# Performance work log

Hardware: AMD Instinct MI355X
Metric: run time of the kernel (lower is better)

Reference implementation:

```python
import jax, jax.numpy as jnp
import numpy as np

G, N, F_IN = 1024, 256, 128
HID = [256, 256, 256]
KS = [32, 16, 8]
N_OUT = 2


def _graph_conv(adj, x, W, b, act):
    # DGL GraphConv, norm='both': h = D^{-1/2} A D^{-1/2} X W + b
    deg = adj.sum(-1)                                   # [G, n]
    norm = jax.lax.rsqrt(jnp.maximum(deg, 1.0))[..., None]
    h = (x * norm) @ W                                  # [G, n, d_out]
    h = jnp.einsum('gnm,gmd->gnd', adj, h) * norm + b
    return act(h) if act is not None else h


def _sag_pool(adj, x, Ws, bs, k):
    # SAGPool: score via GraphConv, keep top-k nodes, gate by tanh(score),
    # take induced subgraph adjacency.
    score = _graph_conv(adj, x, Ws, bs, None)[..., 0]   # [G, n]
    sv, idx = jax.lax.top_k(score, k)                   # [G, k]
    x_sel = jnp.take_along_axis(x, idx[:, :, None], axis=1) * jnp.tanh(sv)[:, :, None]
    a = jnp.take_along_axis(adj, idx[:, :, None], axis=1)
    a = jnp.take_along_axis(a, idx[:, None, :], axis=2)  # [G, k, k]
    return a, x_sel


def _sum_max_readout(x):
    return jnp.concatenate([x.sum(axis=1), x.max(axis=1)], axis=-1)  # [G, 2d]


def setup_inputs() -> dict:
    key = jax.random.key(0)
    ks = jax.random.split(key, 16)
    feat = jax.random.normal(ks[0], (G, N, F_IN), dtype=jnp.float32)
    # sparse-ish symmetric binary adjacency, avg degree ~ 16
    a = (jax.random.uniform(ks[1], (G, N, N)) < (16.0 / N)).astype(jnp.float32)
    adj = jnp.maximum(a, jnp.swapaxes(a, 1, 2))

    def glorot(k, shp):
        lim = float(np.sqrt(6.0 / (shp[0] + shp[1])))
        return jax.random.uniform(k, shp, jnp.float32, -lim, lim)

    dims = [F_IN] + HID
    inp = {'feat': feat, 'adj': adj}
    for i in range(3):
        inp[f'W{i}'] = glorot(ks[2 + i], (dims[i], dims[i + 1]))
        inp[f'b{i}'] = jnp.zeros((dims[i + 1],), jnp.float32)
        inp[f'Ws{i}'] = glorot(ks[5 + i], (dims[i + 1], 1))
        inp[f'bs{i}'] = jnp.zeros((1,), jnp.float32)
    inp['Wd1'] = glorot(ks[8], (2 * sum(HID), 128))
    inp['bd1'] = jnp.zeros((128,), jnp.float32)
    inp['Wd2'] = glorot(ks[9], (128, N_OUT))
    inp['bd2'] = jnp.zeros((N_OUT,), jnp.float32)
    return inp


def reference(feat, adj, W0, b0, Ws0, bs0, W1, b1, Ws1, bs1, W2, b2, Ws2, bs2,
              Wd1, bd1, Wd2, bd2):
    act = jax.nn.leaky_relu  # F.leaky_relu, slope 0.01
    Wgs = [(W0, b0), (W1, b1), (W2, b2)]
    Wss = [(Ws0, bs0), (Ws1, bs1), (Ws2, bs2)]
    readouts = []
    x, a = feat, adj
    for i in range(3):
        x = _graph_conv(a, x, Wgs[i][0], Wgs[i][1], act)
        a, x = _sag_pool(a, x, Wss[i][0], Wss[i][1], KS[i])
        readouts.append(_sum_max_readout(x))
    merged = jnp.concatenate(readouts, axis=1)          # [G, 2*sum(HID)]
    # dropout omitted (deterministic eval reference)
    h = act(merged @ Wd1 + bd1)
    out = jax.nn.sigmoid(h @ Wd2 + bd2)                 # [G, n_output]
    return out
```

## Files before the change

kernel.cpp:

```cpp
#include <hip/hip_runtime.h>
#include <math.h>

constexpr int GG  = 1024;
constexpr int NN  = 256;
constexpr int FF  = 128;
constexpr int DD  = 256;
constexpr int KS0 = 32, KS1 = 16, KS2 = 8;

__device__ __forceinline__ float lrelu(float x){ return x >= 0.f ? x : 0.01f*x; }

__device__ __forceinline__ unsigned short f2bf(float f) {
  unsigned u = __float_as_uint(f);
  unsigned r = (u + 0x7FFFu + ((u >> 16) & 1u)) >> 16;
  return (unsigned short)r;
}
__device__ __forceinline__ float bf2f(unsigned short h) {
  return __uint_as_float(((unsigned)h) << 16);
}

typedef __attribute__((ext_vector_type(8)))  __bf16 bf16x8;
typedef __attribute__((ext_vector_type(16))) float  f32x16;

union Frag8 { unsigned short us[8]; unsigned long long u64[2]; bf16x8 v; };

__global__ void k_splitW(const float* __restrict__ W, unsigned short* __restrict__ out, int K) {
  int e = blockIdx.x*256 + threadIdx.x;
  if (e >= DD*K) return;
  int j    = e & 7;
  int lane = (e >> 3) & 63;
  int nt   = (e >> 9) & 7;
  int s    = (e >> 12) & 1;
  int kti  = e >> 13;
  int n = nt*32 + (lane & 31);
  int k = kti*32 + s*16 + ((lane >> 5) << 3) + j;
  float x = W[(size_t)k*DD + n];
  unsigned short h1 = f2bf(x);  float r1 = x - bf2f(h1);
  unsigned short h2 = f2bf(r1); float r2 = r1 - bf2f(h2);
  unsigned short h3 = f2bf(r2);
  out[e] = h1; out[DD*K + e] = h2; out[2*DD*K + e] = h3;
}

__global__ void k_maskrow(const float* __restrict__ adj, float* __restrict__ norm0,
                          unsigned long long* __restrict__ mask) {
  int row = blockIdx.x*4 + (threadIdx.x >> 6);
  int lane = threadIdx.x & 63;
  const float* ar = adj + (size_t)row*NN;
  float f0 = ar[lane], f1 = ar[64 + lane], f2 = ar[128 + lane], f3 = ar[192 + lane];
  unsigned long long m0 = __ballot(f0 > 0.5f);
  unsigned long long m1 = __ballot(f1 > 0.5f);
  unsigned long long m2 = __ballot(f2 > 0.5f);
  unsigned long long m3 = __ballot(f3 > 0.5f);
  if (lane < 4) {
    unsigned long long mm = lane == 0 ? m0 : lane == 1 ? m1 : lane == 2 ? m2 : m3;
    mask[(size_t)row*4 + lane] = mm;
  }
  if (lane == 0) {
    int cnt = __popcll(m0) + __popcll(m1) + __popcll(m2) + __popcll(m3);
    norm0[row] = rsqrtf(fmaxf((float)cnt, 1.0f));
  }
}

constexpr int QS = 68;
__global__ __launch_bounds__(256, 2) void k_spmm_f(
    const float* __restrict__ feat, const unsigned long long* __restrict__ mask,
    const float* __restrict__ norm0, float* __restrict__ T0) {
  __shared__ unsigned short ls[3*128*QS];
  __shared__ float snorm[NN];

  int g = blockIdx.x;
  int t = threadIdx.x;
  int lane = t & 63, wave = t >> 6;
  int lm = lane & 31, lh = lane >> 5;

  const float* Xg = feat + (size_t)g*NN*FF;

  snorm[t] = norm0[g*NN + t];

  unsigned long long mrow[2][4];
  #pragma unroll
  for (int mt = 0; mt < 2; ++mt) {
    const unsigned long long* mp = mask + ((size_t)g*NN + wave*64 + mt*32 + lm)*4;
    #pragma unroll
    for (int w = 0; w < 4; ++w) mrow[mt][w] = mp[w];
  }

  f32x16 acc[2][4];
  #pragma unroll
  for (int i = 0; i < 2; ++i)
    #pragma unroll
    for (int j = 0; j < 4; ++j) acc[i][j] = (f32x16)0.0f;

  __syncthreads();

  for (int kq = 0; kq < 4; ++kq) {
    #pragma unroll
    for (int i = 0; i < 8; ++i) {
      int g2 = t + i*256;
      int c  = g2 & 127;
      int mg = g2 >> 7;
      int m0 = kq*64 + mg*4;
      unsigned long long p1 = 0, p2 = 0, p3 = 0;
      #pragma unroll
      for (int jj = 0; jj < 4; ++jj) {
        float x = Xg[(size_t)(m0 + jj)*FF + c] * snorm[m0 + jj];
        unsigned short h1 = f2bf(x);  float r1 = x - bf2f(h1);
        unsigned short h2 = f2bf(r1); float r2 = r1 - bf2f(h2);
        unsigned short h3 = f2bf(r2);
        p1 |= (unsigned long long)h1 << (16*jj);
        p2 |= (unsigned long long)h2 << (16*jj);
        p3 |= (unsigned long long)h3 << (16*jj);
      }
      int base = c*QS + mg*4;
      *reinterpret_cast<unsigned long long*>(&ls[base])            = p1;
      *reinterpret_cast<unsigned long long*>(&ls[128*QS + base])   = p2;
      *reinterpret_cast<unsigned long long*>(&ls[2*128*QS + base]) = p3;
    }
    __syncthreads();

    #pragma unroll
    for (int ktq = 0; ktq < 2; ++ktq) {
      Frag8 afr[2][2];
      #pragma unroll
      for (int mt = 0; mt < 2; ++mt)
        #pragma unroll
        for (int s = 0; s < 2; ++s) {
          int shift = ktq*32 + s*16 + lh*8;
          unsigned byte = (unsigned)(mrow[mt][kq] >> shift) & 0xFFu;
          #pragma unroll
          for (int j = 0; j < 8; ++j)
            afr[mt][s].us[j] = ((byte >> j) & 1u) ? (unsigned short)0x3F80 : (unsigned short)0;
        }
      #pragma unroll
      for (int s = 0; s < 2; ++s)
        #pragma unroll
        for (int nt = 0; nt < 4; ++nt) {
          int kk = ktq*32 + s*16 + lh*8;
          int base = (nt*32 + lm)*QS + kk;
          Frag8 b0_, b1_, b2_;
          b0_.v = *reinterpret_cast<const bf16x8*>(&ls[base]);
          b1_.v = *reinterpret_cast<const bf16x8*>(&ls[128*QS + base]);
          b2_.v = *reinterpret_cast<const bf16x8*>(&ls[2*128*QS + base]);
          #pragma unroll
          for (int mt = 0; mt < 2; ++mt) {
            acc[mt][nt] = __builtin_amdgcn_mfma_f32_32x32x16_bf16(afr[mt][s].v, b0_.v, acc[mt][nt], 0,0,0);
            acc[mt][nt] = __builtin_amdgcn_mfma_f32_32x32x16_bf16(afr[mt][s].v, b1_.v, acc[mt][nt], 0,0,0);
            acc[mt][nt] = __builtin_amdgcn_mfma_f32_32x32x16_bf16(afr[mt][s].v, b2_.v, acc[mt][nt], 0,0,0);
          }
        }
    }
    __syncthreads();
  }

  #pragma unroll
  for (int mt = 0; mt < 2; ++mt)
    #pragma unroll
    for (int nt = 0; nt < 4; ++nt)
      #pragma unroll
      for (int r = 0; r < 16; ++r) {
        int row = wave*64 + mt*32 + (r & 3) + 8*(r >> 2) + 4*lh;
        int col = nt*32 + lm;
        T0[((size_t)g*NN + row)*FF + col] = acc[mt][nt][r];
      }
}

__global__ __launch_bounds__(256, 2) void k_gemm0(
    const float* __restrict__ Tmat, const unsigned short* __restrict__ Wk,
    const float* __restrict__ normv, const float* __restrict__ bias,
    const float* __restrict__ Ws, float* __restrict__ hs) {
  __shared__ unsigned short bsh[3*8192];
  int t = threadIdx.x;
  int lane = t & 63, wave = t >> 6;
  int lm = lane & 31, lh = lane >> 5;
  int rowbase = blockIdx.x*128 + wave*32;

  f32x16 acc[8];
  #pragma unroll
  for (int nt = 0; nt < 8; ++nt) acc[nt] = (f32x16)0.0f;

  for (int kti = 0; kti < 4; ++kti) {
    int kt = kti*32;
    float4 af[2][2];
    #pragma unroll
    for (int s = 0; s < 2; ++s) {
      const float* ap = Tmat + (size_t)(rowbase + lm)*FF + kt + s*16 + lh*8;
      af[s][0] = *reinterpret_cast<const float4*>(ap);
      af[s][1] = *reinterpret_cast<const float4*>(ap + 4);
    }
    __syncthreads();
    #pragma unroll
    for (int sp = 0; sp < 3; ++sp)
      #pragma unroll
      for (int r = 0; r < 4; ++r) {
        const uint4* src = reinterpret_cast<const uint4*>(
            Wk + (size_t)sp*DD*FF + (size_t)kti*8192 + r*2048 + t*8);
        *reinterpret_cast<uint4*>(bsh + sp*8192 + r*2048 + t*8) = *src;
      }
    __syncthreads();
    Frag8 afr[2][3];
    #pragma unroll
    for (int s = 0; s < 2; ++s) {
      const float* fv = &af[s][0].x;
      #pragma unroll
      for (int j = 0; j < 8; ++j) {
        float x = fv[j];
        unsigned short h1 = f2bf(x);  float r1 = x - bf2f(h1);
        unsigned short h2 = f2bf(r1); float r2 = r1 - bf2f(h2);
        afr[s][0].us[j] = h1; afr[s][1].us[j] = h2; afr[s][2].us[j] = f2bf(r2);
      }
    }
    #pragma unroll
    for (int s = 0; s < 2; ++s)
      #pragma unroll
      for (int nt = 0; nt < 8; ++nt) {
        const unsigned short* bp = bsh + ((s*8 + nt)*64 + lane)*8;
        Frag8 b0_, b1_, b2_;
        b0_.v = *reinterpret_cast<const bf16x8*>(bp);
        b1_.v = *reinterpret_cast<const bf16x8*>(bp + 8192);
        b2_.v = *reinterpret_cast<const bf16x8*>(bp + 16384);
        acc[nt] = __builtin_amdgcn_mfma_f32_32x32x16_bf16(afr[s][0].v, b0_.v, acc[nt], 0,0,0);
        acc[nt] = __builtin_amdgcn_mfma_f32_32x32x16_bf16(afr[s][0].v, b1_.v, acc[nt], 0,0,0);
        acc[nt] = __builtin_amdgcn_mfma_f32_32x32x16_bf16(afr[s][1].v, b0_.v, acc[nt], 0,0,0);
        acc[nt] = __builtin_amdgcn_mfma_f32_32x32x16_bf16(afr[s][0].v, b2_.v, acc[nt], 0,0,0);
        acc[nt] = __builtin_amdgcn_mfma_f32_32x32x16_bf16(afr[s][2].v, b0_.v, acc[nt], 0,0,0);
        acc[nt] = __builtin_amdgcn_mfma_f32_32x32x16_bf16(afr[s][1].v, b1_.v, acc[nt], 0,0,0);
      }
  }

  float bcol[8], wcol[8];
  #pragma unroll
  for (int nt = 0; nt < 8; ++nt) { int col = nt*32 + lm; bcol[nt] = bias[col]; wcol[nt] = Ws[col]; }
  float hsum[16];
  #pragma unroll
  for (int r = 0; r < 16; ++r) {
    int row = rowbase + (r & 3) + 8*(r >> 2) + 4*lh;
    float nv = normv[row];
    float hp = 0.f;
    #pragma unroll
    for (int nt = 0; nt < 8; ++nt) hp += lrelu(nv*acc[nt][r] + bcol[nt])*wcol[nt];
    hsum[r] = hp;
  }
  #pragma unroll
  for (int off = 1; off <= 16; off <<= 1)
    #pragma unroll
    for (int r = 0; r < 16; ++r) hsum[r] += __shfl_xor(hsum[r], off);
  if (lm == 0)
    #pragma unroll
    for (int r = 0; r < 16; ++r) {
      int row = rowbase + (r & 3) + 8*(r >> 2) + 4*lh;
      hs[row] = normv[row]*hsum[r];
    }
}

template<int K, bool WRITE_X>
__global__ __launch_bounds__(64, 2) void k_gemm_mfma(
    const float* __restrict__ Tmat, const unsigned short* __restrict__ Wk,
    const float* __restrict__ normv, const float* __restrict__ bias,
    const float* __restrict__ Ws, float* __restrict__ xout, float* __restrict__ hs) {
  int lane = threadIdx.x;
  int lm = lane & 31, lh = lane >> 5;
  int rowbase = blockIdx.x * 32;

  f32x16 acc[8];
  #pragma unroll
  for (int nt = 0; nt < 8; ++nt) acc[nt] = (f32x16)0.0f;

  for (int kt = 0; kt < K; kt += 32) {
    float4 af[2][2];
    #pragma unroll
    for (int s = 0; s < 2; ++s) {
      const float* ap = Tmat + (size_t)(rowbase + lm)*K + kt + s*16 + lh*8;
      af[s][0] = *reinterpret_cast<const float4*>(ap);
      af[s][1] = *reinterpret_cast<const float4*>(ap + 4);
    }
    Frag8 afr[2][3];
    #pragma unroll
    for (int s = 0; s < 2; ++s) {
      const float* fv = &af[s][0].x;
      #pragma unroll
      for (int j = 0; j < 8; ++j) {
        float x = fv[j];
        unsigned short h1 = f2bf(x);  float r1 = x - bf2f(h1);
        unsigned short h2 = f2bf(r1); float r2 = r1 - bf2f(h2);
        afr[s][0].us[j] = h1; afr[s][1].us[j] = h2; afr[s][2].us[j] = f2bf(r2);
      }
    }
    #pragma unroll
    for (int s = 0; s < 2; ++s)
      #pragma unroll
      for (int nt = 0; nt < 8; ++nt) {
        size_t boff = ((((size_t)(kt >> 5)*2 + s)*8 + nt)*64 + lane)*8;
        Frag8 b0_, b1_, b2_;
        b0_.v = *reinterpret_cast<const bf16x8*>(Wk + boff);
        b1_.v = *reinterpret_cast<const bf16x8*>(Wk + (size_t)DD*K + boff);
        b2_.v = *reinterpret_cast<const bf16x8*>(Wk + (size_t)2*DD*K + boff);
        acc[nt] = __builtin_amdgcn_mfma_f32_32x32x16_bf16(afr[s][0].v, b0_.v, acc[nt], 0,0,0);
        acc[nt] = __builtin_amdgcn_mfma_f32_32x32x16_bf16(afr[s][0].v, b1_.v, acc[nt], 0,0,0);
        acc[nt] = __builtin_amdgcn_mfma_f32_32x32x16_bf16(afr[s][1].v, b0_.v, acc[nt], 0,0,0);
        acc[nt] = __builtin_amdgcn_mfma_f32_32x32x16_bf16(afr[s][0].v, b2_.v, acc[nt], 0,0,0);
        acc[nt] = __builtin_amdgcn_mfma_f32_32x32x16_bf16(afr[s][2].v, b0_.v, acc[nt], 0,0,0);
        acc[nt] = __builtin_amdgcn_mfma_f32_32x32x16_bf16(afr[s][1].v, b1_.v, acc[nt], 0,0,0);
      }
  }

  float bcol[8], wcol[8];
  #pragma unroll
  for (int nt = 0; nt < 8; ++nt) { int col = nt*32 + lm; bcol[nt] = bias[col]; wcol[nt] = Ws[col]; }
  float hsum[16];
  #pragma unroll
  for (int r = 0; r < 16; ++r) {
    int row = rowbase + (r & 3) + 8*(r >> 2) + 4*lh;
    float nv = normv[row];
    float hp = 0.f;
    #pragma unroll
    for (int nt = 0; nt < 8; ++nt) {
      float val = lrelu(nv*acc[nt][r] + bcol[nt]);
      if (WRITE_X) xout[(size_t)row*DD + nt*32 + lm] = val;
      hp += val*wcol[nt];
    }
    hsum[r] = hp;
  }
  #pragma unroll
  for (int off = 1; off <= 16; off <<= 1)
    #pragma unroll
    for (int r = 0; r < 16; ++r) hsum[r] += __shfl_xor(hsum[r], off);
  if (lm == 0)
    #pragma unroll
    for (int r = 0; r < 16; ++r) {
      int row = rowbase + (r & 3) + 8*(r >> 2) + 4*lh;
      hs[row] = normv[row]*hsum[r];
    }
}

__global__ void k_score_topk0(const unsigned long long* __restrict__ mask,
                              const float* __restrict__ hs, const float* __restrict__ norm0,
                              const float* __restrict__ bs,
                              int* __restrict__ idx_out, float* __restrict__ tv_out) {
  __shared__ float sh[NN];
  __shared__ float ssc[NN];
  int g = blockIdx.x, t = threadIdx.x;
  sh[t] = hs[g*NN + t];
  __syncthreads();
  const unsigned long long* mr = mask + ((size_t)g*NN + t)*4;
  float s = 0.f;
  #pragma unroll
  for (int w = 0; w < 4; ++w) {
    unsigned long long m = mr[w];
    const float* base = sh + w*64;
    while (m) {
      int c = __builtin_ctzll(m);
      s += base[c];
      m &= m - 1;
    }
  }
  ssc[t] = norm0[g*NN + t]*s + bs[0];
  __syncthreads();
  if (t < 64) {
    float sv[4]; int si[4];
    #pragma unroll
    for (int e = 0; e < 4; ++e) { sv[e] = ssc[e*64 + t]; si[e] = e*64 + t; }
    for (int kk = 0; kk < KS0; ++kk) {
      float bs_ = -INFINITY; int bi = 1 << 30;
      #pragma unroll
      for (int e = 0; e < 4; ++e)
        if (sv[e] > bs_ || (sv[e] == bs_ && si[e] < bi)) { bs_ = sv[e]; bi = si[e]; }
      for (int off = 32; off; off >>= 1) {
        float os = __shfl_xor(bs_, off);
        int oi = __shfl_xor(bi, off);
        if (os > bs_ || (os == bs_ && oi < bi)) { bs_ = os; bi = oi; }
      }
      if (t == 0) { idx_out[g*KS0 + kk] = bi; tv_out[g*KS0 + kk] = tanhf(bs_); }
      #pragma unroll
      for (int e = 0; e < 4; ++e) if (si[e] == bi) sv[e] = -INFINITY;
    }
  }
}

__global__ void k_sel0(const float* __restrict__ T0, const float* __restrict__ W0,
                       const float* __restrict__ norm0, const float* __restrict__ b0,
                       const int* __restrict__ idx, const float* __restrict__ tv,
                       const unsigned long long* __restrict__ mask, float* __restrict__ x_sel,
                       float* __restrict__ a1, float* __restrict__ merged) {
  __shared__ float sT[KS0*FF];
  __shared__ int sidx[KS0]; __shared__ float stv[KS0]; __shared__ float snv[KS0];
  int g = blockIdx.x, t = threadIdx.x;
  if (t < KS0) { sidx[t] = idx[g*KS0 + t]; stv[t] = tv[g*KS0 + t]; }
  __syncthreads();
  if (t < KS0) snv[t] = norm0[g*NN + sidx[t]];
  #pragma unroll
  for (int i = 0; i < 16; ++i) {
    int e = t + i*256, r = e >> 7, c = e & 127;
    sT[e] = T0[((size_t)g*NN + sidx[r])*FF + c];
  }
  __syncthreads();
  float sum[KS0];
  #pragma unroll
  for (int j = 0; j < KS0; ++j) sum[j] = 0.f;
  for (int k = 0; k < FF; k += 4) {
    float4 w;
    w.x = W0[(size_t)(k+0)*DD + t]; w.y = W0[(size_t)(k+1)*DD + t];
    w.z = W0[(size_t)(k+2)*DD + t]; w.w = W0[(size_t)(k+3)*DD + t];
    #pragma unroll
    for (int j = 0; j < KS0; ++j) {
      float4 tv4 = *reinterpret_cast<const float4*>(&sT[j*FF + k]);
      sum[j] += tv4.x*w.x + tv4.y*w.y + tv4.z*w.z + tv4.w*w.w;
    }
  }
  float b = b0[t];
  float s = 0.f, mx = -INFINITY;
  #pragma unroll
  for (int j = 0; j < KS0; ++j) {
    float val = lrelu(snv[j]*sum[j] + b) * stv[j];
    x_sel[((size_t)g*KS0 + j)*DD + t] = val;
    s += val; mx = fmaxf(mx, val);
  }
  merged[(size_t)g*1536 + t] = s;
  merged[(size_t)g*1536 + 256 + t] = mx;
  for (int e = t; e < KS0*KS0; e += 256) {
    int r = e >> 5, c = e & 31;
    int nr = sidx[r], nc = sidx[c];
    unsigned long long m = mask[((size_t)g*NN + nr)*4 + (nc >> 6)];
    a1[(size_t)g*KS0*KS0 + e] = (float)((m >> (nc & 63)) & 1ull);
  }
}

template<int n, int k, bool LAST>
__global__ void k_pool(const float* __restrict__ x, const float* __restrict__ a,
                       const float* __restrict__ hs, const float* __restrict__ normv,
                       const float* __restrict__ bs, float* __restrict__ x_sel,
                       float* __restrict__ a_out, float* __restrict__ merged, int moff) {
  __shared__ float sa[n*n];
  __shared__ float shs[n];
  __shared__ float ssc[n];
  __shared__ int sidx[k]; __shared__ float stv[k];
  int g = blockIdx.x, t = threadIdx.x;
  for (int e = t; e < n*n; e += 256) sa[e] = a[(size_t)g*n*n + e];
  if (t < n) shs[t] = hs[g*n + t];
  __syncthreads();
  if (t < n) {
    float s = 0.f;
    #pragma unroll
    for (int m = 0; m < n; ++m) s += sa[t*n + m]*shs[m];
    ssc[t] = normv[g*n + t]*s + bs[0];
  }
  __syncthreads();
  if (t < 64) {
    float sc = (t < n) ? ssc[t] : -INFINITY;
    int si = (t < n) ? t : (1 << 30);
    for (int kk = 0; kk < k; ++kk) {
      float bs_ = sc; int bi = si;
      for (int off = 32; off; off >>= 1) {
        float os = __shfl_xor(bs_, off);
        int oi = __shfl_xor(bi, off);
        if (os > bs_ || (os == bs_ && oi < bi)) { bs_ = os; bi = oi; }
      }
      if (t == 0) { sidx[kk] = bi; stv[kk] = tanhf(bs_); }
      if (si == bi) sc = -INFINITY;
    }
  }
  __syncthreads();
  float sum = 0.f, mx = -INFINITY;
  #pragma unroll
  for (int j = 0; j < k; ++j) {
    float v = x[((size_t)g*n + sidx[j])*DD + t] * stv[j];
    if (!LAST) x_sel[((size_t)g*k + j)*DD + t] = v;
    sum += v; mx = fmaxf(mx, v);
  }
  merged[(size_t)g*1536 + moff + t] = sum;
  merged[(size_t)g*1536 + moff + 256 + t] = mx;
  if (!LAST && t < k*k) {
    int r = t / k, c = t - r*k;
    a_out[(size_t)g*k*k + t] = sa[sidx[r]*n + sidx[c]];
  }
}

template<int n>
__global__ void k_spmm_dense(const float* __restrict__ a, const float* __restrict__ x,
                             float* __restrict__ normv, float* __restrict__ T) {
  __shared__ float sa[n*n];
  __shared__ float snorm[n];
  __shared__ float sx[n*DD];
  int g = blockIdx.x; int t = threadIdx.x;
  for (int e = t; e < n*n; e += 256) sa[e] = a[(size_t)g*n*n + e];
  __syncthreads();
  if (t < n) {
    float dg = 0.f;
    for (int m = 0; m < n; ++m) dg += sa[t*n + m];
    float nv = rsqrtf(fmaxf(dg, 1.f));
    snorm[t] = nv; normv[g*n + t] = nv;
  }
  __syncthreads();
  for (int e = t; e < n*DD; e += 256) sx[e] = x[(size_t)g*n*DD + e] * snorm[e >> 8];
  __syncthreads();
  float acc[n];
  #pragma unroll
  for (int r = 0; r < n; ++r) acc[r] = 0.f;
  for (int m = 0; m < n; ++m) {
    float xv = sx[m*DD + t];
    #pragma unroll
    for (int r = 0; r < n; ++r) acc[r] += sa[r*n + m]*xv;
  }
  for (int r = 0; r < n; ++r) T[((size_t)g*n + r)*DD + t] = acc[r];
}

__global__ void k_mlp(const float* __restrict__ merged, const float* __restrict__ Wd1,
                      const float* __restrict__ bd1, const float* __restrict__ Wd2,
                      const float* __restrict__ bd2, float* __restrict__ out) {
  __shared__ float sm[4*1536];
  __shared__ float sh[4][128];
  int g0 = blockIdx.x*4; int t = threadIdx.x;
  for (int i = t; i < 4*1536; i += 128) sm[i] = merged[(size_t)g0*1536 + i];
  __syncthreads();
  float a0 = 0.f, a1 = 0.f, a2 = 0.f, a3 = 0.f;
  for (int kk = 0; kk < 1536; ++kk) {
    float w = Wd1[(size_t)kk*128 + t];
    a0 += sm[kk]*w; a1 += sm[1536 + kk]*w; a2 += sm[3072 + kk]*w; a3 += sm[4608 + kk]*w;
  }
  float b = bd1[t];
  sh[0][t] = lrelu(a0 + b); sh[1][t] = lrelu(a1 + b);
  sh[2][t] = lrelu(a2 + b); sh[3][t] = lrelu(a3 + b);
  __syncthreads();
  if (t < 8) {
    int gi = t >> 1, c = t & 1;
    float o = 0.f;
    for (int kk = 0; kk < 128; ++kk) o += sh[gi][kk]*Wd2[kk*2 + c];
    out[(size_t)(g0 + gi)*2 + c] = 1.f/(1.f + expf(-(o + bd2[c])));
  }
}

extern "C" void kernel_launch(void* const* d_in, const int* in_sizes, int n_in,
                              void* d_out, int out_size, void* d_ws, size_t ws_size,
                              hipStream_t stream) {
  const float* feat = (const float*)d_in[0];
  const float* adj  = (const float*)d_in[1];
  const float* W0 = (const float*)d_in[2];  const float* b0  = (const float*)d_in[3];
  const float* Ws0= (const float*)d_in[4];  const float* bs0 = (const float*)d_in[5];
  const float* W1 = (const float*)d_in[6];  const float* b1  = (const float*)d_in[7];
  const float* Ws1= (const float*)d_in[8];  const float* bs1 = (const float*)d_in[9];
  const float* W2 = (const float*)d_in[10]; const float* b2  = (const float*)d_in[11];
  const float* Ws2= (const float*)d_in[12]; const float* bs2 = (const float*)d_in[13];
  const float* Wd1= (const float*)d_in[14]; const float* bd1 = (const float*)d_in[15];
  const float* Wd2= (const float*)d_in[16]; const float* bd2 = (const float*)d_in[17];
  float* out = (float*)d_out;

  char* ws = (char*)d_ws;
  size_t off = 0;
  auto alloc = [&](size_t bytes) -> char* {
    char* p = ws + off; off += (bytes + 255) & ~(size_t)255; return p;
  };
  float* norm0 = (float*)alloc((size_t)GG*NN*4);
  unsigned long long* mask0 = (unsigned long long*)alloc((size_t)GG*NN*4*8);
  float* hs0   = (float*)alloc((size_t)GG*NN*4);
  int*   idx0  = (int*)  alloc((size_t)GG*KS0*4);
  float* tv0   = (float*)alloc((size_t)GG*KS0*4);
  float* norm1 = (float*)alloc((size_t)GG*KS0*4);
  float* hs1   = (float*)alloc((size_t)GG*KS0*4);
  float* norm2 = (float*)alloc((size_t)GG*KS1*4);
  float* hs2   = (float*)alloc((size_t)GG*KS1*4);
  float* merged= (float*)alloc((size_t)GG*1536*4);
  unsigned short* W0s = (unsigned short*)alloc((size_t)3*FF*DD*2);
  unsigned short* W1s = (unsigned short*)alloc((size_t)3*DD*DD*2);
  unsigned short* W2s = (unsigned short*)alloc((size_t)3*DD*DD*2);
  char* regA = alloc((size_t)GG*NN*FF*4);
  char* regB = alloc((size_t)GG*160*DD*4);

  float* T0 = (float*)regA;
  float* T1 = (float*)regA;
  float* x_sel1 = (float*)regB;
  float* a1     = (float*)(regB + (size_t)GG*KS0*DD*4);
  float* x2     = (float*)((char*)a1     + (size_t)GG*KS0*KS0*4);
  float* x_sel2 = (float*)((char*)x2     + (size_t)GG*KS0*DD*4);
  float* a2     = (float*)((char*)x_sel2 + (size_t)GG*KS1*DD*4);
  float* T2     = (float*)((char*)a2     + (size_t)GG*KS1*KS1*4);
  float* x3     = (float*)((char*)T2     + (size_t)GG*KS1*DD*4);

  k_splitW<<<(FF*DD + 255)/256, 256, 0, stream>>>(W0, W0s, FF);
  k_splitW<<<(DD*DD + 255)/256, 256, 0, stream>>>(W1, W1s, DD);
  k_splitW<<<(DD*DD + 255)/256, 256, 0, stream>>>(W2, W2s, DD);

  k_maskrow<<<GG*NN/4, 256, 0, stream>>>(adj, norm0, mask0);
  k_spmm_f<<<GG, 256, 0, stream>>>(feat, mask0, norm0, T0);
  k_gemm0<<<GG*NN/128, 256, 0, stream>>>(T0, W0s, norm0, b0, Ws0, hs0);
  k_score_topk0<<<GG, 256, 0, stream>>>(mask0, hs0, norm0, bs0, idx0, tv0);
  k_sel0<<<GG, 256, 0, stream>>>(T0, W0, norm0, b0, idx0, tv0, mask0, x_sel1, a1, merged);

  k_spmm_dense<KS0><<<GG, 256, 0, stream>>>(a1, x_sel1, norm1, T1);
  k_gemm_mfma<DD, true><<<GG*KS0/32, 64, 0, stream>>>(T1, W1s, norm1, b1, Ws1, x2, hs1);
  k_pool<KS0, KS1, false><<<GG, 256, 0, stream>>>(x2, a1, hs1, norm1, bs1, x_sel2, a2, merged, 512);

  k_spmm_dense<KS1><<<GG, 256, 0, stream>>>(a2, x_sel2, norm2, T2);
  k_gemm_mfma<DD, true><<<GG*KS1/32, 64, 0, stream>>>(T2, W2s, norm2, b2, Ws2, x3, hs2);
  k_pool<KS1, KS2, true><<<GG, 256, 0, stream>>>(x3, a2, hs2, norm2, bs2, nullptr, nullptr, merged, 1024);

  k_mlp<<<GG/4, 128, 0, stream>>>(merged, Wd1, bd1, Wd2, bd2, out);

  (void)in_sizes; (void)n_in; (void)out_size; (void)ws_size;
}
```

Before: 1.023 ms.

## Fuse per-graph conv, GEMM, and pooling stages into single kernels

Merges the three weight-split launches into one, fuses top-k scoring with layer-0 selection, and collapses the dense spmm + MFMA GEMM + pool sequence for layers 1 and 2 into one block-per-graph kernel each, keeping intermediates in LDS. It also switches the gemm0 weight staging to async global-to-LDS copies and vectorizes the gather of selected rows. This removes several kernel launches and global round trips for T, x and score buffers. In exchange the fused kernels use large LDS footprints and fewer waves per graph, which may limit occupancy, and the layer-2 MFMA wastes half its rows on padding.

```diff
diff --git a/kernel.cpp b/kernel.cpp
--- a/kernel.cpp
+++ b/kernel.cpp
@@ -23,9 +23,22 @@
 
 union Frag8 { unsigned short us[8]; unsigned long long u64[2]; bf16x8 v; };
 
-__global__ void k_splitW(const float* __restrict__ W, unsigned short* __restrict__ out, int K) {
+typedef __attribute__((address_space(1))) void gvoid;
+typedef __attribute__((address_space(3))) void lvoid;
+__device__ __forceinline__ void async_cp16(const unsigned short* g, unsigned short* l) {
+  __builtin_amdgcn_global_load_lds((const gvoid*)g, (lvoid*)l, 16, 0, 0);
+}
+
+__global__ void k_splitW_all(const float* __restrict__ Wa, const float* __restrict__ Wb,
+                             const float* __restrict__ Wc,
+                             unsigned short* __restrict__ oa, unsigned short* __restrict__ ob,
+                             unsigned short* __restrict__ oc) {
   int e = blockIdx.x*256 + threadIdx.x;
-  if (e >= DD*K) return;
+  if (e >= FF*DD + 2*DD*DD) return;
+  const float* W; unsigned short* out; int K;
+  if (e < FF*DD)                { W = Wa; out = oa; K = FF; }
+  else if (e < FF*DD + DD*DD)   { e -= FF*DD; W = Wb; out = ob; K = DD; }
+  else                          { e -= FF*DD + DD*DD; W = Wc; out = oc; K = DD; }
   int j    = e & 7;
   int lane = (e >> 3) & 63;
   int nt   = (e >> 9) & 7;
@@ -191,9 +204,9 @@
     for (int sp = 0; sp < 3; ++sp)
       #pragma unroll
       for (int r = 0; r < 4; ++r) {
-        const uint4* src = reinterpret_cast<const uint4*>(
-            Wk + (size_t)sp*DD*FF + (size_t)kti*8192 + r*2048 + t*8);
-        *reinterpret_cast<uint4*>(bsh + sp*8192 + r*2048 + t*8) = *src;
+        const unsigned short* src = Wk + (size_t)sp*DD*FF + (size_t)kti*8192 + r*2048 + t*8;
+        unsigned short* dst = bsh + sp*8192 + r*2048 + t*8;
+        async_cp16(src, dst);
       }
     __syncthreads();
     Frag8 afr[2][3];
@@ -251,93 +264,18 @@
     }
 }
 
-template<int K, bool WRITE_X>
-__global__ __launch_bounds__(64, 2) void k_gemm_mfma(
-    const float* __restrict__ Tmat, const unsigned short* __restrict__ Wk,
-    const float* __restrict__ normv, const float* __restrict__ bias,
-    const float* __restrict__ Ws, float* __restrict__ xout, float* __restrict__ hs) {
-  int lane = threadIdx.x;
-  int lm = lane & 31, lh = lane >> 5;
-  int rowbase = blockIdx.x * 32;
-
-  f32x16 acc[8];
-  #pragma unroll
-  for (int nt = 0; nt < 8; ++nt) acc[nt] = (f32x16)0.0f;
-
-  for (int kt = 0; kt < K; kt += 32) {
-    float4 af[2][2];
-    #pragma unroll
-    for (int s = 0; s < 2; ++s) {
-      const float* ap = Tmat + (size_t)(rowbase + lm)*K + kt + s*16 + lh*8;
-      af[s][0] = *reinterpret_cast<const float4*>(ap);
-      af[s][1] = *reinterpret_cast<const float4*>(ap + 4);
-    }
-    Frag8 afr[2][3];
-    #pragma unroll
-    for (int s = 0; s < 2; ++s) {
-      const float* fv = &af[s][0].x;
-      #pragma unroll
-      for (int j = 0; j < 8; ++j) {
-        float x = fv[j];
-        unsigned short h1 = f2bf(x);  float r1 = x - bf2f(h1);
-        unsigned short h2 = f2bf(r1); float r2 = r1 - bf2f(h2);
-        afr[s][0].us[j] = h1; afr[s][1].us[j] = h2; afr[s][2].us[j] = f2bf(r2);
-      }
-    }
-    #pragma unroll
-    for (int s = 0; s < 2; ++s)
-      #pragma unroll
-      for (int nt = 0; nt < 8; ++nt) {
-        size_t boff = ((((size_t)(kt >> 5)*2 + s)*8 + nt)*64 + lane)*8;
-        Frag8 b0_, b1_, b2_;
-        b0_.v = *reinterpret_cast<const bf16x8*>(Wk + boff);
-        b1_.v = *reinterpret_cast<const bf16x8*>(Wk + (size_t)DD*K + boff);
-        b2_.v = *reinterpret_cast<const bf16x8*>(Wk + (size_t)2*DD*K + boff);
-        acc[nt] = __builtin_amdgcn_mfma_f32_32x32x16_bf16(afr[s][0].v, b0_.v, acc[nt], 0,0,0);
-        acc[nt] = __builtin_amdgcn_mfma_f32_32x32x16_bf16(afr[s][0].v, b1_.v, acc[nt], 0,0,0);
-        acc[nt] = __builtin_amdgcn_mfma_f32_32x32x16_bf16(afr[s][1].v, b0_.v, acc[nt], 0,0,0);
-        acc[nt] = __builtin_amdgcn_mfma_f32_32x32x16_bf16(afr[s][0].v, b2_.v, acc[nt], 0,0,0);
-        acc[nt] = __builtin_amdgcn_mfma_f32_32x32x16_bf16(afr[s][2].v, b0_.v, acc[nt], 0,0,0);
-        acc[nt] = __builtin_amdgcn_mfma_f32_32x32x16_bf16(afr[s][1].v, b1_.v, acc[nt], 0,0,0);
-      }
-  }
-
-  float bcol[8], wcol[8];
-  #pragma unroll
-  for (int nt = 0; nt < 8; ++nt) { int col = nt*32 + lm; bcol[nt] = bias[col]; wcol[nt] = Ws[col]; }
-  float hsum[16];
-  #pragma unroll
-  for (int r = 0; r < 16; ++r) {
-    int row = rowbase + (r & 3) + 8*(r >> 2) + 4*lh;
-    float nv = normv[row];
-    float hp = 0.f;
-    #pragma unroll
-    for (int nt = 0; nt < 8; ++nt) {
-      float val = lrelu(nv*acc[nt][r] + bcol[nt]);
-      if (WRITE_X) xout[(size_t)row*DD + nt*32 + lm] = val;
-      hp += val*wcol[nt];
-    }
-    hsum[r] = hp;
-  }
-  #pragma unroll
-  for (int off = 1; off <= 16; off <<= 1)
-    #pragma unroll
-    for (int r = 0; r < 16; ++r) hsum[r] += __shfl_xor(hsum[r], off);
-  if (lm == 0)
-    #pragma unroll
-    for (int r = 0; r < 16; ++r) {
-      int row = rowbase + (r & 3) + 8*(r >> 2) + 4*lh;
-      hs[row] = normv[row]*hsum[r];
-    }
-}
-
-__global__ void k_score_topk0(const unsigned long long* __restrict__ mask,
-                              const float* __restrict__ hs, const float* __restrict__ norm0,
-                              const float* __restrict__ bs,
-                              int* __restrict__ idx_out, float* __restrict__ tv_out) {
+__global__ __launch_bounds__(256) void k_topk_sel0(
+    const unsigned long long* __restrict__ mask, const float* __restrict__ hs,
+    const float* __restrict__ norm0, const float* __restrict__ bs,
+    const float* __restrict__ T0, const float* __restrict__ W0,
+    const float* __restrict__ b0, float* __restrict__ x_sel,
+    float* __restrict__ a1, float* __restrict__ merged) {
   __shared__ float sh[NN];
   __shared__ float ssc[NN];
+  __shared__ float sT[KS0*FF];
+  __shared__ int sidx[KS0]; __shared__ float stv[KS0]; __shared__ float snv[KS0];
   int g = blockIdx.x, t = threadIdx.x;
+
   sh[t] = hs[g*NN + t];
   __syncthreads();
   const unsigned long long* mr = mask + ((size_t)g*NN + t)*4;
@@ -368,28 +306,19 @@
         int oi = __shfl_xor(bi, off);
         if (os > bs_ || (os == bs_ && oi < bi)) { bs_ = os; bi = oi; }
       }
-      if (t == 0) { idx_out[g*KS0 + kk] = bi; tv_out[g*KS0 + kk] = tanhf(bs_); }
+      if (t == 0) { sidx[kk] = bi; stv[kk] = tanhf(bs_); }
       #pragma unroll
       for (int e = 0; e < 4; ++e) if (si[e] == bi) sv[e] = -INFINITY;
     }
   }
-}
-
-__global__ void k_sel0(const float* __restrict__ T0, const float* __restrict__ W0,
-                       const float* __restrict__ norm0, const float* __restrict__ b0,
-                       const int* __restrict__ idx, const float* __restrict__ tv,
-                       const unsigned long long* __restrict__ mask, float* __restrict__ x_sel,
-                       float* __restrict__ a1, float* __restrict__ merged) {
-  __shared__ float sT[KS0*FF];
-  __shared__ int sidx[KS0]; __shared__ float stv[KS0]; __shared__ float snv[KS0];
-  int g = blockIdx.x, t = threadIdx.x;
-  if (t < KS0) { sidx[t] = idx[g*KS0 + t]; stv[t] = tv[g*KS0 + t]; }
   __syncthreads();
   if (t < KS0) snv[t] = norm0[g*NN + sidx[t]];
   #pragma unroll
-  for (int i = 0; i < 16; ++i) {
-    int e = t + i*256, r = e >> 7, c = e & 127;
-    sT[e] = T0[((size_t)g*NN + sidx[r])*FF + c];
+  for (int i = 0; i < 4; ++i) {
+    int e4 = t + i*256;
+    int r = e4 >> 5, c4 = e4 & 31;
+    reinterpret_cast<float4*>(sT)[e4] =
+        *reinterpret_cast<const float4*>(&T0[((size_t)g*NN + sidx[r])*FF + c4*4]);
   }
   __syncthreads();
   float sum[KS0];
@@ -406,14 +335,14 @@
     }
   }
   float b = b0[t];
-  float s = 0.f, mx = -INFINITY;
+  float ssum = 0.f, mx = -INFINITY;
   #pragma unroll
   for (int j = 0; j < KS0; ++j) {
     float val = lrelu(snv[j]*sum[j] + b) * stv[j];
     x_sel[((size_t)g*KS0 + j)*DD + t] = val;
-    s += val; mx = fmaxf(mx, val);
-  }
-  merged[(size_t)g*1536 + t] = s;
+    ssum += val; mx = fmaxf(mx, val);
+  }
+  merged[(size_t)g*1536 + t] = ssum;
   merged[(size_t)g*1536 + 256 + t] = mx;
   for (int e = t; e < KS0*KS0; e += 256) {
     int r = e >> 5, c = e & 31;
@@ -423,30 +352,142 @@
   }
 }
 
-template<int n, int k, bool LAST>
-__global__ void k_pool(const float* __restrict__ x, const float* __restrict__ a,
-                       const float* __restrict__ hs, const float* __restrict__ normv,
-                       const float* __restrict__ bs, float* __restrict__ x_sel,
-                       float* __restrict__ a_out, float* __restrict__ merged, int moff) {
+__global__ __launch_bounds__(256, 2) void k_fused1(
+    const float* __restrict__ a, const float* __restrict__ xin,
+    const unsigned short* __restrict__ Wk, const float* __restrict__ bias,
+    const float* __restrict__ Ws, const float* __restrict__ bs,
+    float* __restrict__ x_sel_out, float* __restrict__ a_out,
+    float* __restrict__ merged) {
+  constexpr int n = KS0;
+  constexpr int kp = KS1;
+  constexpr int TP = DD + 4;
   __shared__ float sa[n*n];
-  __shared__ float shs[n];
-  __shared__ float ssc[n];
-  __shared__ int sidx[k]; __shared__ float stv[k];
+  __shared__ float bufA[n*DD];
+  __shared__ float sT[n*TP];
+  __shared__ float snorm[n]; __shared__ float shs[n]; __shared__ float ssc[n];
+  __shared__ int sidx[kp]; __shared__ float stv[kp];
   int g = blockIdx.x, t = threadIdx.x;
+  int lane = t & 63, wave = t >> 6, lm = lane & 31, lh = lane >> 5;
+
   for (int e = t; e < n*n; e += 256) sa[e] = a[(size_t)g*n*n + e];
-  if (t < n) shs[t] = hs[g*n + t];
+  __syncthreads();
+  if (t < n) {
+    float dg = 0.f;
+    for (int m = 0; m < n; ++m) dg += sa[m*n + t];
+    snorm[t] = rsqrtf(fmaxf(dg, 1.f));
+  }
+  __syncthreads();
+  {
+    const float4* xp = reinterpret_cast<const float4*>(xin + (size_t)g*n*DD);
+    #pragma unroll
+    for (int i = 0; i < (n*DD/4)/256; ++i) {
+      int e4 = t + i*256;
+      float4 v = xp[e4];
+      float nv = snorm[e4 >> 6];
+      v.x *= nv; v.y *= nv; v.z *= nv; v.w *= nv;
+      reinterpret_cast<float4*>(bufA)[e4] = v;
+    }
+  }
+  __syncthreads();
+  {
+    float acc2[n];
+    #pragma unroll
+    for (int r = 0; r < n; ++r) acc2[r] = 0.f;
+    for (int m = 0; m < n; ++m) {
+      float xv = bufA[m*DD + t];
+      #pragma unroll
+      for (int r = 0; r < n; ++r) acc2[r] += sa[r*n + m]*xv;
+    }
+    #pragma unroll
+    for (int r = 0; r < n; ++r) sT[r*TP + t] = acc2[r];
+  }
+  __syncthreads();
+
+  f32x16 acc[2];
+  acc[0] = (f32x16)0.0f; acc[1] = (f32x16)0.0f;
+  for (int kti = 0; kti < DD/32; ++kti) {
+    int kt = kti*32;
+    Frag8 afr[2][3];
+    #pragma unroll
+    for (int s = 0; s < 2; ++s) {
+      float4 af4[2];
+      const float* ap = &sT[lm*TP + kt + s*16 + lh*8];
+      af4[0] = *reinterpret_cast<const float4*>(ap);
+      af4[1] = *reinterpret_cast<const float4*>(ap + 4);
+      const float* fv = &af4[0].x;
+      #pragma unroll
+      for (int j = 0; j < 8; ++j) {
+        float x = fv[j];
+        unsigned short h1 = f2bf(x);  float r1 = x - bf2f(h1);
+        unsigned short h2 = f2bf(r1); float r2 = r1 - bf2f(h2);
+        afr[s][0].us[j] = h1; afr[s][1].us[j] = h2; afr[s][2].us[j] = f2bf(r2);
+      }
+    }
+    #pragma unroll
+    for (int s = 0; s < 2; ++s)
+      #pragma unroll
+      for (int ntl = 0; ntl < 2; ++ntl) {
+        int ct = wave*2 + ntl;
+        size_t boff = ((((size_t)kti*2 + s)*8 + ct)*64 + lane)*8;
+        Frag8 b0_, b1_, b2_;
+        b0_.v = *reinterpret_cast<const bf16x8*>(Wk + boff);
+        b1_.v = *reinterpret_cast<const bf16x8*>(Wk + (size_t)DD*DD + boff);
+        b2_.v = *reinterpret_cast<const bf16x8*>(Wk + (size_t)2*DD*DD + boff);
+        acc[ntl] = __builtin_amdgcn_mfma_f32_32x32x16_bf16(afr[s][0].v, b0_.v, acc[ntl], 0,0,0);
+        acc[ntl] = __builtin_amdgcn_mfma_f32_32x32x16_bf16(afr[s][0].v, b1_.v, acc[ntl], 0,0,0);
+        acc[ntl] = __builtin_amdgcn_mfma_f32_32x32x16_bf16(afr[s][1].v, b0_.v, acc[ntl], 0,0,0);
+        acc[ntl] = __builtin_amdgcn_mfma_f32_32x32x16_bf16(afr[s][0].v, b2_.v, acc[ntl], 0,0,0);
+        acc[ntl] = __builtin_amdgcn_mfma_f32_32x32x16_bf16(afr[s][2].v, b0_.v, acc[ntl], 0,0,0);
+        acc[ntl] = __builtin_amdgcn_mfma_f32_32x32x16_bf16(afr[s][1].v, b1_.v, acc[ntl], 0,0,0);
+      }
+  }
+
+  #pragma unroll
+  for (int ntl = 0; ntl < 2; ++ntl) {
+    int colbase = wave*64 + ntl*32 + lm;
+    float bc = bias[colbase];
+    #pragma unroll
+    for (int r = 0; r < 16; ++r) {
+      int row = (r & 3) + 8*(r >> 2) + 4*lh;
+      bufA[row*DD + colbase] = lrelu(snorm[row]*acc[ntl][r] + bc);
+    }
+  }
+  __syncthreads();
+  if (wave == 0) {
+    float wcol[8];
+    #pragma unroll
+    for (int nt = 0; nt < 8; ++nt) wcol[nt] = Ws[nt*32 + lm];
+    float hsum[16];
+    #pragma unroll
+    for (int r = 0; r < 16; ++r) {
+      int row = (r & 3) + 8*(r >> 2) + 4*lh;
+      float hp = 0.f;
+      #pragma unroll
+      for (int nt = 0; nt < 8; ++nt) hp += bufA[row*DD + nt*32 + lm]*wcol[nt];
+      hsum[r] = hp;
+    }
+    #pragma unroll
+    for (int off = 1; off <= 16; off <<= 1)
+      #pragma unroll
+      for (int r = 0; r < 16; ++r) hsum[r] += __shfl_xor(hsum[r], off);
+    if (lm == 0)
+      #pragma unroll
+      for (int r = 0; r < 16; ++r) {
+        int row = (r & 3) + 8*(r >> 2) + 4*lh;
+        shs[row] = snorm[row]*hsum[r];
+      }
+  }
   __syncthreads();
   if (t < n) {
     float s = 0.f;
-    #pragma unroll
-    for (int m = 0; m < n; ++m) s += sa[t*n + m]*shs[m];
-    ssc[t] = normv[g*n + t]*s + bs[0];
+    for (int m = 0; m < n; ++m) s += sa[m*n + t]*shs[m];
+    ssc[t] = snorm[t]*s + bs[0];
   }
   __syncthreads();
   if (t < 64) {
     float sc = (t < n) ? ssc[t] : -INFINITY;
     int si = (t < n) ? t : (1 << 30);
-    for (int kk = 0; kk < k; ++kk) {
+    for (int kk = 0; kk < kp; ++kk) {
       float bs_ = sc; int bi = si;
       for (int off = 32; off; off >>= 1) {
         float os = __shfl_xor(bs_, off);
@@ -460,46 +501,178 @@
   __syncthreads();
   float sum = 0.f, mx = -INFINITY;
   #pragma unroll
-  for (int j = 0; j < k; ++j) {
-    float v = x[((size_t)g*n + sidx[j])*DD + t] * stv[j];
-    if (!LAST) x_sel[((size_t)g*k + j)*DD + t] = v;
+  for (int j = 0; j < kp; ++j) {
+    float v = bufA[sidx[j]*DD + t] * stv[j];
+    x_sel_out[((size_t)g*kp + j)*DD + t] = v;
     sum += v; mx = fmaxf(mx, v);
   }
-  merged[(size_t)g*1536 + moff + t] = sum;
-  merged[(size_t)g*1536 + moff + 256 + t] = mx;
-  if (!LAST && t < k*k) {
-    int r = t / k, c = t - r*k;
-    a_out[(size_t)g*k*k + t] = sa[sidx[r]*n + sidx[c]];
-  }
-}
-
-template<int n>
-__global__ void k_spmm_dense(const float* __restrict__ a, const float* __restrict__ x,
-                             float* __restrict__ normv, float* __restrict__ T) {
+  merged[(size_t)g*1536 + 512 + t] = sum;
+  merged[(size_t)g*1536 + 768 + t] = mx;
+  { int r = t >> 4, c = t & 15;
+    a_out[(size_t)g*kp*kp + t] = sa[sidx[r]*n + sidx[c]]; }
+}
+
+__global__ __launch_bounds__(256, 2) void k_fused2(
+    const float* __restrict__ a, const float* __restrict__ xin,
+    const unsigned short* __restrict__ Wk, const float* __restrict__ bias,
+    const float* __restrict__ Ws, const float* __restrict__ bs,
+    float* __restrict__ merged) {
+  constexpr int n = KS1;
+  constexpr int kp = KS2;
+  constexpr int TP = DD + 4;
   __shared__ float sa[n*n];
-  __shared__ float snorm[n];
-  __shared__ float sx[n*DD];
-  int g = blockIdx.x; int t = threadIdx.x;
+  __shared__ float bufA[n*DD];
+  __shared__ float sT[n*TP];
+  __shared__ float snorm[n]; __shared__ float shs[n]; __shared__ float ssc[n];
+  __shared__ int sidx[kp]; __shared__ float stv[kp];
+  int g = blockIdx.x, t = threadIdx.x;
+  int lane = t & 63, wave = t >> 6, lm = lane & 31, lh = lane >> 5;
+
   for (int e = t; e < n*n; e += 256) sa[e] = a[(size_t)g*n*n + e];
   __syncthreads();
   if (t < n) {
     float dg = 0.f;
-    for (int m = 0; m < n; ++m) dg += sa[t*n + m];
-    float nv = rsqrtf(fmaxf(dg, 1.f));
-    snorm[t] = nv; normv[g*n + t] = nv;
-  }
-  __syncthreads();
-  for (int e = t; e < n*DD; e += 256) sx[e] = x[(size_t)g*n*DD + e] * snorm[e >> 8];
-  __syncthreads();
-  float acc[n];
-  #pragma unroll
-  for (int r = 0; r < n; ++r) acc[r] = 0.f;
-  for (int m = 0; m < n; ++m) {
-    float xv = sx[m*DD + t];
-    #pragma unroll
-    for (int r = 0; r < n; ++r) acc[r] += sa[r*n + m]*xv;
-  }
-  for (int r = 0; r < n; ++r) T[((size_t)g*n + r)*DD + t] = acc[r];
+    for (int m = 0; m < n; ++m) dg += sa[m*n + t];
+    snorm[t] = rsqrtf(fmaxf(dg, 1.f));
+  }
+  __syncthreads();
+  {
+    const float4* xp = reinterpret_cast<const float4*>(xin + (size_t)g*n*DD);
+    #pragma unroll
+    for (int i = 0; i < (n*DD/4)/256; ++i) {
+      int e4 = t + i*256;
+      float4 v = xp[e4];
+      float nv = snorm[e4 >> 6];
+      v.x *= nv; v.y *= nv; v.z *= nv; v.w *= nv;
+      reinterpret_cast<float4*>(bufA)[e4] = v;
+    }
+  }
+  __syncthreads();
+  {
+    float acc2[n];
+    #pragma unroll
+    for (int r = 0; r < n; ++r) acc2[r] = 0.f;
+    for (int m = 0; m < n; ++m) {
+      float xv = bufA[m*DD + t];
+      #pragma unroll
+      for (int r = 0; r < n; ++r) acc2[r] += sa[r*n + m]*xv;
+    }
+    #pragma unroll
+    for (int r = 0; r < n; ++r) sT[r*TP + t] = acc2[r];
+  }
+  __syncthreads();
+
+  f32x16 acc[2];
+  acc[0] = (f32x16)0.0f; acc[1] = (f32x16)0.0f;
+  for (int kti = 0; kti < DD/32; ++kti) {
+    int kt = kti*32;
+    Frag8 afr[2][3];
+    #pragma unroll
+    for (int s = 0; s < 2; ++s) {
+      float4 af4[2];
+      if (lm < n) {
+        const float* ap = &sT[lm*TP + kt + s*16 + lh*8];
+        af4[0] = *reinterpret_cast<const float4*>(ap);
+        af4[1] = *reinterpret_cast<const float4*>(ap + 4);
+      } else {
+        af4[0] = make_float4(0.f, 0.f, 0.f, 0.f);
+        af4[1] = make_float4(0.f, 0.f, 0.f, 0.f);
+      }
+      const float* fv = &af4[0].x;
+      #pragma unroll
+      for (int j = 0; j < 8; ++j) {
+        float x = fv[j];
+        unsigned short h1 = f2bf(x);  float r1 = x - bf2f(h1);
+        unsigned short h2 = f2bf(r1); float r2 = r1 - bf2f(h2);
+        afr[s][0].us[j] = h1; afr[s][1].us[j] = h2; afr[s][2].us[j] = f2bf(r2);
+      }
+    }
+    #pragma unroll
+    for (int s = 0; s < 2; ++s)
+      #pragma unroll
+      for (int ntl = 0; ntl < 2; ++ntl) {
+        int ct = wave*2 + ntl;
+        size_t boff = ((((size_t)kti*2 + s)*8 + ct)*64 + lane)*8;
+        Frag8 b0_, b1_, b2_;
+        b0_.v = *reinterpret_cast<const bf16x8*>(Wk + boff);
+        b1_.v = *reinterpret_cast<const bf16x8*>(Wk + (size_t)DD*DD + boff);
+        b2_.v = *reinterpret_cast<const bf16x8*>(Wk + (size_t)2*DD*DD + boff);
+        acc[ntl] = __builtin_amdgcn_mfma_f32_32x32x16_bf16(afr[s][0].v, b0_.v, acc[ntl], 0,0,0);
+        acc[ntl] = __builtin_amdgcn_mfma_f32_32x32x16_bf16(afr[s][0].v, b1_.v, acc[ntl], 0,0,0);
+        acc[ntl] = __builtin_amdgcn_mfma_f32_32x32x16_bf16(afr[s][1].v, b0_.v, acc[ntl], 0,0,0);
+        acc[ntl] = __builtin_amdgcn_mfma_f32_32x32x16_bf16(afr[s][0].v, b2_.v, acc[ntl], 0,0,0);
+        acc[ntl] = __builtin_amdgcn_mfma_f32_32x32x16_bf16(afr[s][2].v, b0_.v, acc[ntl], 0,0,0);
+        acc[ntl] = __builtin_amdgcn_mfma_f32_32x32x16_bf16(afr[s][1].v, b1_.v, acc[ntl], 0,0,0);
+      }
+  }
+
+  #pragma unroll
+  for (int ntl = 0; ntl < 2; ++ntl) {
+    int colbase = wave*64 + ntl*32 + lm;
+    float bc = bias[colbase];
+    #pragma unroll
+    for (int r = 0; r < 16; ++r) {
+      int row = (r & 3) + 8*(r >> 2) + 4*lh;
+      if (row < n) bufA[row*DD + colbase] = lrelu(snorm[row]*acc[ntl][r] + bc);
+    }
+  }
+  __syncthreads();
+  if (wave == 0) {
+    float wcol[8];
+    #pragma unroll
+    for (int nt = 0; nt < 8; ++nt) wcol[nt] = Ws[nt*32 + lm];
+    float hsum[16];
+    #pragma unroll
+    for (int r = 0; r < 16; ++r) {
+      int row = (r & 3) + 8*(r >> 2) + 4*lh;
+      float hp = 0.f;
+      if (row < n) {
+        #pragma unroll
+        for (int nt = 0; nt < 8; ++nt) hp += bufA[row*DD + nt*32 + lm]*wcol[nt];
+      }
+      hsum[r] = hp;
+    }
+    #pragma unroll
+    for (int off = 1; off <= 16; off <<= 1)
+      #pragma unroll
+      for (int r = 0; r < 16; ++r) hsum[r] += __shfl_xor(hsum[r], off);
+    if (lm == 0)
+      #pragma unroll
+      for (int r = 0; r < 16; ++r) {
+        int row = (r & 3) + 8*(r >> 2) + 4*lh;
+        if (row < n) shs[row] = snorm[row]*hsum[r];
+      }
+  }
+  __syncthreads();
+  if (t < n) {
+    float s = 0.f;
+    for (int m = 0; m < n; ++m) s += sa[m*n + t]*shs[m];
+    ssc[t] = snorm[t]*s + bs[0];
+  }
+  __syncthreads();
+  if (t < 64) {
+    float sc = (t < n) ? ssc[t] : -INFINITY;
+    int si = (t < n) ? t : (1 << 30);
+    for (int kk = 0; kk < kp; ++kk) {
+      float bs_ = sc; int bi = si;
+      for (int off = 32; off; off >>= 1) {
+        float os = __shfl_xor(bs_, off);
+        int oi = __shfl_xor(bi, off);
+        if (os > bs_ || (os == bs_ && oi < bi)) { bs_ = os; bi = oi; }
+      }
+      if (t == 0) { sidx[kk] = bi; stv[kk] = tanhf(bs_); }
+      if (si == bi) sc = -INFINITY;
+    }
+  }
+  __syncthreads();
+  float sum = 0.f, mx = -INFINITY;
+  #pragma unroll
+  for (int j = 0; j < kp; ++j) {
+    float v = bufA[sidx[j]*DD + t] * stv[j];
+    sum += v; mx = fmaxf(mx, v);
+  }
+  merged[(size_t)g*1536 + 1024 + t] = sum;
+  merged[(size_t)g*1536 + 1280 + t] = mx;
 }
 
 __global__ void k_mlp(const float* __restrict__ merged, const float* __restrict__ Wd1,
@@ -550,46 +723,26 @@
   float* norm0 = (float*)alloc((size_t)GG*NN*4);
   unsigned long long* mask0 = (unsigned long long*)alloc((size_t)GG*NN*4*8);
   float* hs0   = (float*)alloc((size_t)GG*NN*4);
-  int*   idx0  = (int*)  alloc((size_t)GG*KS0*4);
-  float* tv0   = (float*)alloc((size_t)GG*KS0*4);
-  float* norm1 = (float*)alloc((size_t)GG*KS0*4);
-  float* hs1   = (float*)alloc((size_t)GG*KS0*4);
-  float* norm2 = (float*)alloc((size_t)GG*KS1*4);
-  float* hs2   = (float*)alloc((size_t)GG*KS1*4);
   float* merged= (float*)alloc((size_t)GG*1536*4);
   unsigned short* W0s = (unsigned short*)alloc((size_t)3*FF*DD*2);
   unsigned short* W1s = (unsigned short*)alloc((size_t)3*DD*DD*2);
   unsigned short* W2s = (unsigned short*)alloc((size_t)3*DD*DD*2);
-  char* regA = alloc((size_t)GG*NN*FF*4);
-  char* regB = alloc((size_t)GG*160*DD*4);
-
-  float* T0 = (float*)regA;
-  float* T1 = (float*)regA;
-  float* x_sel1 = (float*)regB;
-  float* a1     = (float*)(regB + (size_t)GG*KS0*DD*4);
-  float* x2     = (float*)((char*)a1     + (size_t)GG*KS0*KS0*4);
-  float* x_sel2 = (float*)((char*)x2     + (size_t)GG*KS0*DD*4);
-  float* a2     = (float*)((char*)x_sel2 + (size_t)GG*KS1*DD*4);
-  float* T2     = (float*)((char*)a2     + (size_t)GG*KS1*KS1*4);
-  float* x3     = (float*)((char*)T2     + (size_t)GG*KS1*DD*4);
-
-  k_splitW<<<(FF*DD + 255)/256, 256, 0, stream>>>(W0, W0s, FF);
-  k_splitW<<<(DD*DD + 255)/256, 256, 0, stream>>>(W1, W1s, DD);
-  k_splitW<<<(DD*DD + 255)/256, 256, 0, stream>>>(W2, W2s, DD);
+  float* T0     = (float*)alloc((size_t)GG*NN*FF*4);
+  float* x_sel1 = (float*)alloc((size_t)GG*KS0*DD*4);
+  float* a1     = (float*)alloc((size_t)GG*KS0*KS0*4);
+  float* x_sel2 = (float*)alloc((size_t)GG*KS1*DD*4);
+  float* a2     = (float*)alloc((size_t)GG*KS1*KS1*4);
+
+  k_splitW_all<<<(FF*DD + 2*DD*DD)/256, 256, 0, stream>>>(W0, W1, W2, W0s, W1s, W2s);
 
   k_maskrow<<<GG*NN/4, 256, 0, stream>>>(adj, norm0, mask0);
   k_spmm_f<<<GG, 256, 0, stream>>>(feat, mask0, norm0, T0);
   k_gemm0<<<GG*NN/128, 256, 0, stream>>>(T0, W0s, norm0, b0, Ws0, hs0);
-  k_score_topk0<<<GG, 256, 0, stream>>>(mask0, hs0, norm0, bs0, idx0, tv0);
-  k_sel0<<<GG, 256, 0, stream>>>(T0, W0, norm0, b0, idx0, tv0, mask0, x_sel1, a1, merged);
-
-  k_spmm_dense<KS0><<<GG, 256, 0, stream>>>(a1, x_sel1, norm1, T1);
-  k_gemm_mfma<DD, true><<<GG*KS0/32, 64, 0, stream>>>(T1, W1s, norm1, b1, Ws1, x2, hs1);
-  k_pool<KS0, KS1, false><<<GG, 256, 0, stream>>>(x2, a1, hs1, norm1, bs1, x_sel2, a2, merged, 512);
-
-  k_spmm_dense<KS1><<<GG, 256, 0, stream>>>(a2, x_sel2, norm2, T2);
-  k_gemm_mfma<DD, true><<<GG*KS1/32, 64, 0, stream>>>(T2, W2s, norm2, b2, Ws2, x3, hs2);
-  k_pool<KS1, KS2, true><<<GG, 256, 0, stream>>>(x3, a2, hs2, norm2, bs2, nullptr, nullptr, merged, 1024);
+  k_topk_sel0<<<GG, 256, 0, stream>>>(mask0, hs0, norm0, bs0, T0, W0, b0, x_sel1, a1, merged);
+
+  k_fused1<<<GG, 256, 0, stream>>>(a1, x_sel1, W1s, b1, Ws1, bs1, x_sel2, a2, merged);
+
+  k_fused2<<<GG, 256, 0, stream>>>(a2, x_sel2, W2s, b2, Ws2, bs2, merged);
 
   k_mlp<<<GG/4, 128, 0, stream>>>(merged, Wd1, bd1, Wd2, bd2, out);
 
```

Result: faster. 966.2 us (-5.5%).
